# Kernel tuning notes

Measured on AMD Instinct MI355X. Metric: run time of the kernel, lower is better.

The kernel has to match this reference:

```python
import jax, jax.numpy as jnp
import numpy as np

B, C, N, H = 4, 256, 1024, 8
D = C            # per-head q/k dim (out_channels defaults to in_channels)
DV = C           # per-head value/output dim (y_out_channels defaults to out_channels)


def setup_inputs() -> dict:
    key = jax.random.key(0)
    ks = jax.random.split(key, 10)
    s = 0.02
    return {
        "x": jax.random.normal(ks[0], (B, C, N), jnp.float32),
        "y": jax.random.normal(ks[1], (B, C, N), jnp.float32),
        "Wq": jax.random.normal(ks[2], (H * D, C), jnp.float32) * s,
        "bq": jnp.zeros((H * D,), jnp.float32),
        "Wk": jax.random.normal(ks[3], (H * D, C), jnp.float32) * s,
        "bk": jnp.zeros((H * D,), jnp.float32),
        "Wv": jax.random.normal(ks[4], (H * DV, C), jnp.float32) * s,
        "bv": jnp.zeros((H * DV,), jnp.float32),
        "Wp": jax.random.normal(ks[5], (DV, C), jnp.float32) * s,  # projection, bias=False
        "gamma": jax.random.uniform(ks[6], (H, 1, 1, 1), jnp.float32) + 0.001,
    }


def _pconv(t, W, b):
    # 1x1 conv1d: (O,C) x (B,C,N) -> (B,O,N)
    out = jnp.einsum('oc,bcn->bon', W, t)
    return out if b is None else out + b[None, :, None]


def reference(x, y, Wq, bq, Wk, bk, Wv, bv, Wp, gamma):
    b_, _, n_ = x.shape
    h = gamma.shape[0]
    # Q/K/V projections, split channels into h heads (head-major chunks of D)
    q = _pconv(x, Wq, bq).reshape(b_, h, -1, n_)   # [B,H,D,N]
    k = _pconv(x, Wk, bk).reshape(b_, h, -1, n_)   # [B,H,D,N]
    v = _pconv(y, Wv, bv).reshape(b_, h, -1, n_)   # [B,H,DV,N]
    # energy[i,j] = sum_d q[d,i]*k[d,j]; softmax over keys j (no sqrt(d) scaling)
    attn = jax.nn.softmax(jnp.einsum('bhdn,bhdm->bhnm', q, k), axis=-1)
    out = jnp.einsum('bhdm,bhnm->bhdn', v, attn)   # [B,H,DV,N]
    # residual branch: y projected to DV channels (1x1 conv, no bias)
    yp = jnp.einsum('oc,bcn->bon', Wp, y)          # [B,DV,N]
    g = gamma.reshape(1, h, 1, 1)
    out = (g * out + yp[:, None, :, :]) / (1.0 + g)
    # concat heads along channel dim (head-major), matching split_cat(out,1,0,2)
    return out.reshape(b_, -1, n_)                 # [B,H*DV,N]
```

## Files before the change

### kernel.cpp

```cpp
#include <hip/hip_runtime.h>

#define Bb 4
#define Cc 256
#define Nn 1024
#define Hh 8
#define Oo 2048

typedef __attribute__((ext_vector_type(8))) short bf16x8;
typedef __attribute__((ext_vector_type(4))) float f32x4;

__device__ __forceinline__ short f2bf(float f) {
  unsigned u = __builtin_bit_cast(unsigned, f);
  unsigned r = u + 0x7FFFu + ((u >> 16) & 1u);
  return (short)(r >> 16);
}
__device__ __forceinline__ f32x4 mfma16(bf16x8 a, bf16x8 b, f32x4 c) {
  return __builtin_amdgcn_mfma_f32_16x16x32_bf16(a, b, c, 0, 0, 0);
}
__device__ __forceinline__ void gl_lds16(const void* g, void* l) {
  __builtin_amdgcn_global_load_lds(
      (const __attribute__((address_space(1))) void*)g,
      (__attribute__((address_space(3))) void*)l, 16, 0, 0);
}

__device__ __forceinline__ void stage_row512(const char* gbase, char* lds,
                                             int wave, int lane) {
#pragma unroll
  for (int i = 0; i < 8; i++) {
    int off = (wave * 8 + i) * 1024;
    int L = off + lane * 16;
    int r = L >> 9;
    int c = ((L >> 4) & 31) ^ (r & 7);
    gl_lds16(gbase + r * 512 + c * 16, lds + off);
  }
}
__device__ __forceinline__ void stage_v(const char* Vg, char* lds, int k0,
                                        int wave, int lane) {
#pragma unroll
  for (int i = 0; i < 8; i++) {
    int off = (wave * 8 + i) * 1024;
    int L = off + lane * 16;
    int r = L >> 7;
    int c = ((L >> 4) & 7) ^ (r & 7);
    gl_lds16(Vg + (size_t)r * 2048 + k0 * 2 + c * 16, lds + off);
  }
}

__global__ __launch_bounds__(256) void k_transpose(
    const float* __restrict__ x, const float* __restrict__ y,
    short* __restrict__ xT, short* __restrict__ yT,
    const float* __restrict__ Wq, const float* __restrict__ Wk,
    const float* __restrict__ Wv, const float* __restrict__ Wp,
    short* __restrict__ dWq, short* __restrict__ dWk, short* __restrict__ dWv,
    short* __restrict__ dWp) {
  {
    const int NW = Oo * Cc;
    int lin = blockIdx.x + 16 * (blockIdx.y + 4 * blockIdx.z);
    for (int i = (lin * 256 + threadIdx.x) * 4; i < 3 * NW + Cc * Cc;
         i += 512 * 256 * 4) {
      const float* src;
      short* dst;
      int off;
      if (i < NW) {
        src = Wq; dst = dWq; off = i;
      } else if (i < 2 * NW) {
        src = Wk; dst = dWk; off = i - NW;
      } else if (i < 3 * NW) {
        src = Wv; dst = dWv; off = i - 2 * NW;
      } else {
        src = Wp; dst = dWp; off = i - 3 * NW;
      }
      float4 v = *(const float4*)(src + off);
      short4 o;
      o.x = f2bf(v.x);
      o.y = f2bf(v.y);
      o.z = f2bf(v.z);
      o.w = f2bf(v.w);
      *(short4*)(dst + off) = o;
    }
  }
  int bz = blockIdx.z;
  int b = bz >> 1;
  const float* src = (bz & 1) ? y : x;
  short* dst = (bz & 1) ? yT : xT;
  src += (size_t)b * Cc * Nn;
  dst += (size_t)b * Nn * Cc;
  __shared__ short tile[64][72];
  int n0 = blockIdx.x * 64, c0 = blockIdx.y * 64;
  int t = threadIdx.x;
#pragma unroll
  for (int i = 0; i < 16; i++) {
    int idx = t + i * 256;
    int cc = idx >> 6, nn = idx & 63;
    tile[cc][nn] = f2bf(src[(size_t)(c0 + cc) * Nn + n0 + nn]);
  }
  __syncthreads();
#pragma unroll
  for (int i = 0; i < 16; i++) {
    int idx = t + i * 256;
    int nn = idx >> 6, cc = idx & 63;
    dst[(size_t)(n0 + nn) * Cc + c0 + cc] = tile[cc][nn];
  }
}

__global__ __launch_bounds__(256) void k_proj(
    const short* __restrict__ xT, const short* __restrict__ yT,
    const short* __restrict__ Wq, const float* __restrict__ bq,
    const short* __restrict__ Wk, const float* __restrict__ bk,
    const short* __restrict__ Wv, const float* __restrict__ bv,
    const short* __restrict__ Wp, short* __restrict__ Qt,
    short* __restrict__ Kt, short* __restrict__ Vv, float* __restrict__ yp) {
  int wave = threadIdx.x >> 6, lane = threadIdx.x & 63;
  int quad = lane >> 4, l16 = lane & 15;
  int sw = l16 & 7;
  __shared__ short S1[64 * 256];
  __shared__ short S2[64 * 256];
  int id = blockIdx.x;

  if (id < 256) {
    int ot = id >> 3, b = (id >> 1) & 3, nhalf = id & 1;
    int o0 = ot * 64;
    stage_row512((const char*)(Wq + (size_t)o0 * Cc), (char*)S1, wave, lane);
    stage_row512((const char*)(Wk + (size_t)o0 * Cc), (char*)S2, wave, lane);
    float vbq[4], vbk[4];
#pragma unroll
    for (int cj = 0; cj < 4; cj++) {
      vbq[cj] = bq[o0 + cj * 16 + l16];
      vbk[cj] = bk[o0 + cj * 16 + l16];
    }
    const short* xbase = xT + (size_t)b * Nn * Cc;
    bf16x8 areg[8], aregN[8];
    {
      const short* ap =
          xbase + (size_t)(nhalf * 512 + wave * 16 + l16) * Cc + quad * 8;
#pragma unroll
      for (int ks = 0; ks < 8; ks++) areg[ks] = *(const bf16x8*)(ap + ks * 32);
    }
    __syncthreads();
#pragma unroll 1
    for (int i = 0; i < 8; i++) {
      int ncur = nhalf * 512 + i * 64;
      if (i < 7) {
        const short* ap =
            xbase + (size_t)(ncur + 64 + wave * 16 + l16) * Cc + quad * 8;
#pragma unroll
        for (int ks = 0; ks < 8; ks++)
          aregN[ks] = *(const bf16x8*)(ap + ks * 32);
      }
      f32x4 accQ[4], accK[4];
#pragma unroll
      for (int j = 0; j < 4; j++) {
        accQ[j] = f32x4{0.f, 0.f, 0.f, 0.f};
        accK[j] = f32x4{0.f, 0.f, 0.f, 0.f};
      }
#pragma unroll
      for (int ks = 0; ks < 8; ks++) {
#pragma unroll
        for (int cj = 0; cj < 4; cj++) {
          int off = (cj * 16 + l16) * 512 + (((ks * 4 + quad) ^ sw) << 4);
          bf16x8 wqf = *(const bf16x8*)((const char*)S1 + off);
          bf16x8 wkf = *(const bf16x8*)((const char*)S2 + off);
          accQ[cj] = mfma16(areg[ks], wqf, accQ[cj]);
          accK[cj] = mfma16(areg[ks], wkf, accK[cj]);
        }
      }
#pragma unroll
      for (int cj = 0; cj < 4; cj++) {
        int o = o0 + cj * 16 + l16;
        int h = o >> 8, d = o & 255;
#pragma unroll
        for (int r = 0; r < 4; r++) {
          int n = ncur + wave * 16 + quad * 4 + r;
          size_t idx = (((size_t)(b * Hh + h) * Nn) + n) * 256 + d;
          Qt[idx] = f2bf(accQ[cj][r] + vbq[cj]);
          Kt[idx] = f2bf(accK[cj][r] + vbk[cj]);
        }
      }
#pragma unroll
      for (int ks = 0; ks < 8; ks++) areg[ks] = aregN[ks];
    }
  } else {
    int id2 = id - 256;
    int nt = id2 >> 4, b = (id2 >> 2) & 3, oq = id2 & 3;
    int n0 = nt * 64;
    stage_row512((const char*)(yT + (size_t)b * Nn * Cc + (size_t)n0 * Cc),
                 (char*)S1, wave, lane);
    bf16x8 areg[8], aregN[8];
    {
      int ot = oq * 9;
      const short* wb = (ot < 32) ? (Wv + (size_t)ot * 64 * Cc)
                                  : (Wp + (size_t)(ot - 32) * 64 * Cc);
      const short* ap = wb + (size_t)(wave * 16 + l16) * Cc + quad * 8;
#pragma unroll
      for (int ks = 0; ks < 8; ks++) areg[ks] = *(const bf16x8*)(ap + ks * 32);
    }
    __syncthreads();
#pragma unroll 1
    for (int j = 0; j < 9; j++) {
      int ot = oq * 9 + j;
      bool isP = ot >= 32;
      int o0 = (isP ? ot - 32 : ot) * 64;
      if (j < 8) {
        int otn = ot + 1;
        const short* wb = (otn < 32) ? (Wv + (size_t)otn * 64 * Cc)
                                     : (Wp + (size_t)(otn - 32) * 64 * Cc);
        const short* ap = wb + (size_t)(wave * 16 + l16) * Cc + quad * 8;
#pragma unroll
        for (int ks = 0; ks < 8; ks++)
          aregN[ks] = *(const bf16x8*)(ap + ks * 32);
      }
      float4 bvv = *(const float4*)&bv[o0 + wave * 16 + quad * 4];
      f32x4 acc[4];
#pragma unroll
      for (int jj = 0; jj < 4; jj++) acc[jj] = f32x4{0.f, 0.f, 0.f, 0.f};
#pragma unroll
      for (int ks = 0; ks < 8; ks++) {
#pragma unroll
        for (int cj = 0; cj < 4; cj++) {
          bf16x8 bb = *(const bf16x8*)((const char*)S1 + (cj * 16 + l16) * 512 +
                                       (((ks * 4 + quad) ^ sw) << 4));
          acc[cj] = mfma16(areg[ks], bb, acc[cj]);
        }
      }
#pragma unroll
      for (int cj = 0; cj < 4; cj++) {
        int n = n0 + cj * 16 + l16;
#pragma unroll
        for (int r = 0; r < 4; r++) {
          int o = o0 + wave * 16 + quad * 4 + r;
          if (isP) {
            yp[((size_t)b * Cc + o) * Nn + n] = acc[cj][r];
          } else {
            float bvr = (r == 0) ? bvv.x : (r == 1) ? bvv.y : (r == 2) ? bvv.z : bvv.w;
            Vv[((size_t)b * Oo + o) * Nn + n] = f2bf(acc[cj][r] + bvr);
          }
        }
      }
#pragma unroll
      for (int ks = 0; ks < 8; ks++) areg[ks] = aregN[ks];
    }
  }
}

__global__ __launch_bounds__(256) void k_attn(
    const short* __restrict__ Qt, const short* __restrict__ Kt,
    const short* __restrict__ Vv, const float* __restrict__ yp,
    const float* __restrict__ gamma, float* __restrict__ out) {
  int id = blockIdx.x;
  int bh = (id & 7) * 4 + (id >> 7);
  int q0 = ((id >> 3) & 15) * 64;
  int b = bh >> 3, h = bh & 7;
  int wave = threadIdx.x >> 6, lane = threadIdx.x & 63;
  int quad = lane >> 4, l16 = lane & 15;
  int sw = l16 & 7;
  int qh = wave & 1, kh = wave >> 1;
  const short* Qb = Qt + (size_t)bh * Nn * 256;
  const char* Kg = (const char*)(Kt + (size_t)bh * Nn * 256);
  const char* Vg = (const char*)(Vv + (size_t)bh * 256 * Nn);

  __shared__ short Klds[64 * 256];
  __shared__ short Vlds[256 * 64];
  __shared__ short plds[64][64];
  __shared__ float llds[2][64];

  bf16x8 qreg[2][8];
#pragma unroll
  for (int qb2 = 0; qb2 < 2; qb2++) {
    const short* qp =
        Qb + (size_t)(q0 + qh * 32 + qb2 * 16 + l16) * 256 + quad * 8;
#pragma unroll
    for (int ks = 0; ks < 8; ks++)
      qreg[qb2][ks] = *(const bf16x8*)(qp + ks * 32);
  }
  f32x4 oacc[16];
#pragma unroll
  for (int j = 0; j < 16; j++) oacc[j] = f32x4{0.f, 0.f, 0.f, 0.f};
  float l_i[2][4] = {{0.f, 0.f, 0.f, 0.f}, {0.f, 0.f, 0.f, 0.f}};

  stage_row512(Kg, (char*)Klds, wave, lane);
  stage_v(Vg, (char*)Vlds, 0, wave, lane);

  for (int kt = 0; kt < 16; kt++) {
    int k0 = kt * 64;
    __syncthreads();
    f32x4 sc[2][2];
#pragma unroll
    for (int a = 0; a < 2; a++)
#pragma unroll
      for (int c = 0; c < 2; c++) sc[a][c] = f32x4{0.f, 0.f, 0.f, 0.f};
#pragma unroll
    for (int ks = 0; ks < 8; ks++) {
      int chnk = ((ks * 4 + quad) ^ sw) << 4;
      bf16x8 kb0 =
          *(const bf16x8*)((const char*)Klds + (kh * 32 + l16) * 512 + chnk);
      bf16x8 kb1 = *(const bf16x8*)((const char*)Klds +
                                    (kh * 32 + 16 + l16) * 512 + chnk);
      sc[0][0] = mfma16(qreg[0][ks], kb0, sc[0][0]);
      sc[0][1] = mfma16(qreg[0][ks], kb1, sc[0][1]);
      sc[1][0] = mfma16(qreg[1][ks], kb0, sc[1][0]);
      sc[1][1] = mfma16(qreg[1][ks], kb1, sc[1][1]);
    }
#pragma unroll
    for (int qb2 = 0; qb2 < 2; qb2++) {
#pragma unroll
      for (int cj2 = 0; cj2 < 2; cj2++) {
#pragma unroll
        for (int r = 0; r < 4; r++) {
          float p = __expf(sc[qb2][cj2][r]);
          l_i[qb2][r] += p;
          int row = qh * 32 + qb2 * 16 + quad * 4 + r;
          int key = kh * 32 + cj2 * 16 + l16;
          plds[row][((((key >> 3) ^ (row & 7))) << 3) | (key & 7)] = f2bf(p);
        }
      }
    }
    __syncthreads();
    if (kt < 15)
      stage_row512(Kg + (size_t)(k0 + 64) * 512, (char*)Klds, wave, lane);
    bf16x8 ap0[4], ap1[4];
#pragma unroll
    for (int qb = 0; qb < 4; qb++) {
      ap0[qb] = *(const bf16x8*)&plds[qb * 16 + l16][(quad ^ sw) << 3];
      ap1[qb] = *(const bf16x8*)&plds[qb * 16 + l16][((quad + 4) ^ sw) << 3];
    }
#pragma unroll
    for (int dj = 0; dj < 4; dj++) {
      const char* vrow = (const char*)Vlds + (wave * 64 + dj * 16 + l16) * 128;
      bf16x8 v0 = *(const bf16x8*)(vrow + ((quad ^ sw) << 4));
      bf16x8 v1 = *(const bf16x8*)(vrow + (((quad + 4) ^ sw) << 4));
#pragma unroll
      for (int qb = 0; qb < 4; qb++) {
        oacc[qb * 4 + dj] = mfma16(ap0[qb], v0, oacc[qb * 4 + dj]);
        oacc[qb * 4 + dj] = mfma16(ap1[qb], v1, oacc[qb * 4 + dj]);
      }
    }
    __syncthreads();
    if (kt < 15) stage_v(Vg, (char*)Vlds, k0 + 64, wave, lane);
  }
#pragma unroll
  for (int qb2 = 0; qb2 < 2; qb2++) {
#pragma unroll
    for (int r = 0; r < 4; r++) {
      float v = l_i[qb2][r];
      v += __shfl_xor(v, 1);
      v += __shfl_xor(v, 2);
      v += __shfl_xor(v, 4);
      v += __shfl_xor(v, 8);
      l_i[qb2][r] = v;
    }
  }
  if (l16 == 0) {
#pragma unroll
    for (int qb2 = 0; qb2 < 2; qb2++) {
      f32x4 lv;
#pragma unroll
      for (int r = 0; r < 4; r++) lv[r] = l_i[qb2][r];
      *(f32x4*)&llds[kh][qh * 32 + qb2 * 16 + quad * 4] = lv;
    }
  }
  __syncthreads();
  float gf = gamma[h];
  float sg = gf / (1.f + gf), sy = 1.f / (1.f + gf);
#pragma unroll
  for (int qb = 0; qb < 4; qb++) {
    f32x4 lv0 = *(const f32x4*)&llds[0][qb * 16 + quad * 4];
    f32x4 lv1 = *(const f32x4*)&llds[1][qb * 16 + quad * 4];
    int qq = q0 + qb * 16 + quad * 4;
#pragma unroll
    for (int dj = 0; dj < 4; dj++) {
      int dv = wave * 64 + dj * 16 + l16;
      const float* ypp = yp + ((size_t)b * 256 + dv) * Nn + qq;
      float* op = out + ((size_t)b * Oo + h * 256 + dv) * Nn + qq;
      float4 yv = *(const float4*)ypp;
      f32x4 oa = oacc[qb * 4 + dj];
      float4 ov;
      ov.x = sg * (oa[0] / (lv0[0] + lv1[0])) + sy * yv.x;
      ov.y = sg * (oa[1] / (lv0[1] + lv1[1])) + sy * yv.y;
      ov.z = sg * (oa[2] / (lv0[2] + lv1[2])) + sy * yv.z;
      ov.w = sg * (oa[3] / (lv0[3] + lv1[3])) + sy * yv.w;
      *(float4*)op = ov;
    }
  }
}

extern "C" void kernel_launch(void* const* d_in, const int* in_sizes, int n_in,
                              void* d_out, int out_size, void* d_ws,
                              size_t ws_size, hipStream_t stream) {
  const float* x = (const float*)d_in[0];
  const float* y = (const float*)d_in[1];
  const float* Wq = (const float*)d_in[2];
  const float* bq = (const float*)d_in[3];
  const float* Wk = (const float*)d_in[4];
  const float* bk = (const float*)d_in[5];
  const float* Wv = (const float*)d_in[6];
  const float* bv = (const float*)d_in[7];
  const float* Wp = (const float*)d_in[8];
  const float* gamma = (const float*)d_in[9];
  float* out = (float*)d_out;

  char* w = (char*)d_ws;
  short* Qt = (short*)(w + 0);
  short* Kt = (short*)(w + 16777216);
  short* Vv = (short*)(w + 33554432);
  short* xT = (short*)(w + 50331648);
  short* yT = (short*)(w + 52428800);
  float* yp = (float*)(w + 54525952);
  short* Wqb = (short*)(w + 58720256);
  short* Wkb = (short*)(w + 59768832);
  short* Wvb = (short*)(w + 60817408);
  short* Wpb = (short*)(w + 61865984);

  k_transpose<<<dim3(Nn / 64, Cc / 64, 2 * Bb), dim3(256), 0, stream>>>(
      x, y, xT, yT, Wq, Wk, Wv, Wp, Wqb, Wkb, Wvb, Wpb);
  k_proj<<<dim3(512), dim3(256), 0, stream>>>(
      xT, yT, Wqb, bq, Wkb, bk, Wvb, bv, Wpb, Qt, Kt, Vv, yp);
  k_attn<<<dim3(512), dim3(256), 0, stream>>>(Qt, Kt, Vv, yp, gamma, out);
}
```

Before: 207.2 us.

## Give each wave 16 full query rows in QK^T instead of a 2x2 split

The QK^T stage used to split the 64x64 score tile 2x2 across waves: each wave held 32 queries and 32 keys, and the row sums were combined across key halves through LDS. Now each wave owns 16 query rows against all 64 keys. That halves Q register usage and removes the cross-wave row-sum merge. In exchange each wave reads all 64 K rows from LDS per k-step, so K LDS traffic per MFMA doubles relative to Q reuse.

```diff
diff --git a/kernel.cpp b/kernel.cpp
--- a/kernel.cpp
+++ b/kernel.cpp
@@ -253,29 +253,25 @@
   int wave = threadIdx.x >> 6, lane = threadIdx.x & 63;
   int quad = lane >> 4, l16 = lane & 15;
   int sw = l16 & 7;
-  int qh = wave & 1, kh = wave >> 1;
   const short* Qb = Qt + (size_t)bh * Nn * 256;
   const char* Kg = (const char*)(Kt + (size_t)bh * Nn * 256);
   const char* Vg = (const char*)(Vv + (size_t)bh * 256 * Nn);
 
   __shared__ short Klds[64 * 256];
   __shared__ short Vlds[256 * 64];
-  __shared__ short plds[64][64];
-  __shared__ float llds[2][64];
-
-  bf16x8 qreg[2][8];
-#pragma unroll
-  for (int qb2 = 0; qb2 < 2; qb2++) {
-    const short* qp =
-        Qb + (size_t)(q0 + qh * 32 + qb2 * 16 + l16) * 256 + quad * 8;
-#pragma unroll
-    for (int ks = 0; ks < 8; ks++)
-      qreg[qb2][ks] = *(const bf16x8*)(qp + ks * 32);
+  __shared__ short plds[4][16][64];
+  __shared__ float llds[64];
+
+  bf16x8 qreg[8];
+  {
+    const short* qp = Qb + (size_t)(q0 + wave * 16 + l16) * 256 + quad * 8;
+#pragma unroll
+    for (int ks = 0; ks < 8; ks++) qreg[ks] = *(const bf16x8*)(qp + ks * 32);
   }
   f32x4 oacc[16];
 #pragma unroll
   for (int j = 0; j < 16; j++) oacc[j] = f32x4{0.f, 0.f, 0.f, 0.f};
-  float l_i[2][4] = {{0.f, 0.f, 0.f, 0.f}, {0.f, 0.f, 0.f, 0.f}};
+  float l_i[4] = {0.f, 0.f, 0.f, 0.f};
 
   stage_row512(Kg, (char*)Klds, wave, lane);
   stage_v(Vg, (char*)Vlds, 0, wave, lane);
@@ -283,35 +279,28 @@
   for (int kt = 0; kt < 16; kt++) {
     int k0 = kt * 64;
     __syncthreads();
-    f32x4 sc[2][2];
-#pragma unroll
-    for (int a = 0; a < 2; a++)
-#pragma unroll
-      for (int c = 0; c < 2; c++) sc[a][c] = f32x4{0.f, 0.f, 0.f, 0.f};
+    f32x4 sc[4];
+#pragma unroll
+    for (int j = 0; j < 4; j++) sc[j] = f32x4{0.f, 0.f, 0.f, 0.f};
 #pragma unroll
     for (int ks = 0; ks < 8; ks++) {
-      int chnk = ((ks * 4 + quad) ^ sw) << 4;
-      bf16x8 kb0 =
-          *(const bf16x8*)((const char*)Klds + (kh * 32 + l16) * 512 + chnk);
-      bf16x8 kb1 = *(const bf16x8*)((const char*)Klds +
-                                    (kh * 32 + 16 + l16) * 512 + chnk);
-      sc[0][0] = mfma16(qreg[0][ks], kb0, sc[0][0]);
-      sc[0][1] = mfma16(qreg[0][ks], kb1, sc[0][1]);
-      sc[1][0] = mfma16(qreg[1][ks], kb0, sc[1][0]);
-      sc[1][1] = mfma16(qreg[1][ks], kb1, sc[1][1]);
-    }
-#pragma unroll
-    for (int qb2 = 0; qb2 < 2; qb2++) {
-#pragma unroll
-      for (int cj2 = 0; cj2 < 2; cj2++) {
-#pragma unroll
-        for (int r = 0; r < 4; r++) {
-          float p = __expf(sc[qb2][cj2][r]);
-          l_i[qb2][r] += p;
-          int row = qh * 32 + qb2 * 16 + quad * 4 + r;
-          int key = kh * 32 + cj2 * 16 + l16;
-          plds[row][((((key >> 3) ^ (row & 7))) << 3) | (key & 7)] = f2bf(p);
-        }
+#pragma unroll
+      for (int cj = 0; cj < 4; cj++) {
+        bf16x8 kb = *(const bf16x8*)((const char*)Klds +
+                                     (cj * 16 + l16) * 512 +
+                                     (((ks * 4 + quad) ^ sw) << 4));
+        sc[cj] = mfma16(qreg[ks], kb, sc[cj]);
+      }
+    }
+#pragma unroll
+    for (int cj = 0; cj < 4; cj++) {
+#pragma unroll
+      for (int r = 0; r < 4; r++) {
+        float p = __expf(sc[cj][r]);
+        l_i[r] += p;
+        int row = quad * 4 + r;
+        plds[wave][row][(((cj * 2 + (l16 >> 3)) ^ (row & 7)) << 3) | sw] =
+            f2bf(p);
       }
     }
     __syncthreads();
@@ -320,8 +309,8 @@
     bf16x8 ap0[4], ap1[4];
 #pragma unroll
     for (int qb = 0; qb < 4; qb++) {
-      ap0[qb] = *(const bf16x8*)&plds[qb * 16 + l16][(quad ^ sw) << 3];
-      ap1[qb] = *(const bf16x8*)&plds[qb * 16 + l16][((quad + 4) ^ sw) << 3];
+      ap0[qb] = *(const bf16x8*)&plds[qb][l16][(quad ^ sw) << 3];
+      ap1[qb] = *(const bf16x8*)&plds[qb][l16][((quad + 4) ^ sw) << 3];
     }
 #pragma unroll
     for (int dj = 0; dj < 4; dj++) {
@@ -338,33 +327,26 @@
     if (kt < 15) stage_v(Vg, (char*)Vlds, k0 + 64, wave, lane);
   }
 #pragma unroll
-  for (int qb2 = 0; qb2 < 2; qb2++) {
-#pragma unroll
-    for (int r = 0; r < 4; r++) {
-      float v = l_i[qb2][r];
-      v += __shfl_xor(v, 1);
-      v += __shfl_xor(v, 2);
-      v += __shfl_xor(v, 4);
-      v += __shfl_xor(v, 8);
-      l_i[qb2][r] = v;
-    }
+  for (int r = 0; r < 4; r++) {
+    float v = l_i[r];
+    v += __shfl_xor(v, 1);
+    v += __shfl_xor(v, 2);
+    v += __shfl_xor(v, 4);
+    v += __shfl_xor(v, 8);
+    l_i[r] = v;
   }
   if (l16 == 0) {
-#pragma unroll
-    for (int qb2 = 0; qb2 < 2; qb2++) {
-      f32x4 lv;
-#pragma unroll
-      for (int r = 0; r < 4; r++) lv[r] = l_i[qb2][r];
-      *(f32x4*)&llds[kh][qh * 32 + qb2 * 16 + quad * 4] = lv;
-    }
+    f32x4 lv;
+#pragma unroll
+    for (int r = 0; r < 4; r++) lv[r] = l_i[r];
+    *(f32x4*)&llds[wave * 16 + quad * 4] = lv;
   }
   __syncthreads();
   float gf = gamma[h];
   float sg = gf / (1.f + gf), sy = 1.f / (1.f + gf);
 #pragma unroll
   for (int qb = 0; qb < 4; qb++) {
-    f32x4 lv0 = *(const f32x4*)&llds[0][qb * 16 + quad * 4];
-    f32x4 lv1 = *(const f32x4*)&llds[1][qb * 16 + quad * 4];
+    f32x4 lv = *(const f32x4*)&llds[qb * 16 + quad * 4];
     int qq = q0 + qb * 16 + quad * 4;
 #pragma unroll
     for (int dj = 0; dj < 4; dj++) {
@@ -374,10 +356,10 @@
       float4 yv = *(const float4*)ypp;
       f32x4 oa = oacc[qb * 4 + dj];
       float4 ov;
-      ov.x = sg * (oa[0] / (lv0[0] + lv1[0])) + sy * yv.x;
-      ov.y = sg * (oa[1] / (lv0[1] + lv1[1])) + sy * yv.y;
-      ov.z = sg * (oa[2] / (lv0[2] + lv1[2])) + sy * yv.z;
-      ov.w = sg * (oa[3] / (lv0[3] + lv1[3])) + sy * yv.w;
+      ov.x = sg * (oa[0] / lv[0]) + sy * yv.x;
+      ov.y = sg * (oa[1] / lv[1]) + sy * yv.y;
+      ov.z = sg * (oa[2] / lv[2]) + sy * yv.z;
+      ov.w = sg * (oa[3] / lv[3]) + sy * yv.w;
       *(float4*)op = ov;
     }
   }
```

New measurement: 187.7 us. 9.4% less time.
